# Optimization experiments

Measured on AMD Instinct MI355X. Metric: run time of the kernel, lower is better.

The kernel has to match this reference:

```python
import jax, jax.numpy as jnp
import numpy as np

N_NODES = 50000
N_EDGES = 800000
IN_FEATS = 128
OUT_FEATS = 128
HEADS = 2
EW_DIMS = 2
NEG_SLOPE = 0.2


def setup_inputs() -> dict:
    key = jax.random.key(0)
    ks = jax.random.split(key, 8)
    feat = jax.random.normal(ks[0], (N_NODES, IN_FEATS), dtype=jnp.float32)
    e_w = jax.random.uniform(ks[1], (N_EDGES, EW_DIMS), dtype=jnp.float32)
    src = jax.random.randint(ks[2], (N_EDGES,), 0, N_NODES)
    dst = jax.random.randint(ks[3], (N_EDGES,), 0, N_NODES)
    # Learned params: per-head fc weight, attn vectors (xavier-ish scale)
    s = 1.0 / np.sqrt(IN_FEATS)
    W = jax.random.normal(ks[4], (HEADS, OUT_FEATS, IN_FEATS), dtype=jnp.float32) * s
    attn_l = jax.random.normal(ks[5], (HEADS, OUT_FEATS), dtype=jnp.float32) * s
    attn_r = jax.random.normal(ks[6], (HEADS, OUT_FEATS), dtype=jnp.float32) * s
    attn_ew = jax.random.normal(ks[7], (HEADS, EW_DIMS), dtype=jnp.float32)
    return {"feat": feat, "e_w": e_w, "src": src, "dst": dst,
            "W": W, "attn_l": attn_l, "attn_r": attn_r, "attn_ew": attn_ew}


def reference(feat, e_w, src, dst, W, attn_l, attn_r, attn_ew):
    N = feat.shape[0]
    # per-head projection: [N, H, O]
    ft = jnp.einsum('nf,hof->nho', feat, W)
    el = jnp.einsum('nho,ho->nh', ft, attn_l)           # [N, H]
    er = jnp.einsum('nho,ho->nh', ft, attn_r)           # [N, H]
    ew = jnp.einsum('ed,hd->eh', e_w, attn_ew)          # [E, H]
    # u_add_v + edge-weight attention + leaky_relu
    e = jax.nn.leaky_relu(el[src] + er[dst] + ew, NEG_SLOPE)  # [E, H]
    # edge_softmax grouped by destination node (numerically stable)
    emax = jax.ops.segment_max(e, dst, num_segments=N)
    emax = jnp.where(jnp.isfinite(emax), emax, 0.0)
    ee = jnp.exp(e - emax[dst])
    denom = jax.ops.segment_sum(ee, dst, num_segments=N)
    a = ee / jnp.where(denom[dst] > 0, denom[dst], 1.0)       # [E, H]
    # u_mul_e / sum aggregation: [N, H, O]
    m = ft[src] * a[:, :, None]
    rst = jax.ops.segment_sum(m, dst, num_segments=N)
    # residual (Identity since in_feats == out_feats) + elu, then cat heads
    rst = jax.nn.elu(rst + feat[:, None, :])
    return rst.reshape(N, -1)
```

## Files before the change

### kernel.cpp

```cpp
#include <hip/hip_runtime.h>
#include <math.h>

#define NNODES 50000
#define NEDGES 800000
#define INF 128
#define OUTF 128
#define HEADS 2
#define NEG_SLOPE 0.2f

#define CAP 32
#define SCAP 16
#define OVFCAP 32768

__device__ __forceinline__ unsigned short f2bf(float f) {
    unsigned u = __float_as_uint(f);
    unsigned r = (u + 0x7FFFu + ((u >> 16) & 1u)) >> 16;
    return (unsigned short)r;
}
__device__ __forceinline__ float bf2f(unsigned short b) {
    return __uint_as_float((unsigned)b << 16);
}

typedef __attribute__((ext_vector_type(8))) short frag_ab;
typedef __attribute__((ext_vector_type(4))) float frag_cd;
typedef __attribute__((ext_vector_type(8))) unsigned short ushort8v;

#define APITCH 136

__global__ void init_kernel(int* cursor, int* ovfcnt,
                            const float* __restrict__ W,
                            const float* __restrict__ attn_l,
                            const float* __restrict__ attn_r,
                            unsigned short* __restrict__ Wb,
                            float* __restrict__ wfold, int N) {
    const int b = blockIdx.x, t = threadIdx.x;
    const int czblk = (2 * N + 255) >> 8;
    if (b < czblk) {
        int i = b * 256 + t;
        if (i < 2 * N) cursor[i] = 0;
        if (i == 0) *ovfcnt = 0;
        return;
    }
    if (b == czblk) {
        int h = t >> 7, f = t & 127;
        float sl = 0.f, sr = 0.f;
#pragma unroll 16
        for (int o = 0; o < 128; ++o) {
            float wv = W[(size_t)(h * 128 + o) * 128 + f];
            sl = fmaf(attn_l[h * 128 + o], wv, sl);
            sr = fmaf(attn_r[h * 128 + o], wv, sr);
        }
        wfold[h * 128 + f] = sl;
        wfold[(2 + h) * 128 + f] = sr;
        return;
    }
    int base = (b - czblk - 1) * 4096 + t * 16;
#pragma unroll
    for (int q = 0; q < 4; ++q) {
        float4 g = *(const float4*)(W + base + q * 4);
        ushort4 v; v.x = f2bf(g.x); v.y = f2bf(g.y); v.z = f2bf(g.z); v.w = f2bf(g.w);
        *(ushort4*)(Wb + base + q * 4) = v;
    }
}

__global__ __launch_bounds__(256) void gemm_mfma(const float* __restrict__ feat,
                                                 const unsigned short* __restrict__ Wb,
                                                 const float* __restrict__ wfold,
                                                 unsigned short* __restrict__ ftb,
                                                 float* __restrict__ el,
                                                 float* __restrict__ er,
                                                 int N) {
    __shared__ unsigned short Bs[256 * APITCH];
    const int t = threadIdx.x;
    const int w = t >> 6, lane = t & 63;
    const int m16 = lane & 15, quad = lane >> 4;
    const int n0 = blockIdx.x * 64;
    const int r = n0 + w * 16 + m16;
    const bool valid = r < N;

#pragma unroll
    for (int i = 0; i < 16; ++i) {
        int q = t + i * 256;
        int row = q >> 4, c = q & 15;
        ushort8v v = *(const ushort8v*)(Wb + row * 128 + c * 8);
        *(ushort8v*)(&Bs[row * APITCH + c * 8]) = v;
    }

    frag_ab af[4];
    float pd[4] = {0.f, 0.f, 0.f, 0.f};
#pragma unroll
    for (int kc = 0; kc < 4; ++kc) {
        const int cc = kc * 32 + quad * 8;
        float4 g0 = make_float4(0.f, 0.f, 0.f, 0.f), g1 = g0;
        if (valid) {
            g0 = *(const float4*)(feat + (size_t)r * INF + cc);
            g1 = *(const float4*)(feat + (size_t)r * INF + cc + 4);
        }
        frag_ab a;
        a[0] = (short)f2bf(g0.x); a[1] = (short)f2bf(g0.y);
        a[2] = (short)f2bf(g0.z); a[3] = (short)f2bf(g0.w);
        a[4] = (short)f2bf(g1.x); a[5] = (short)f2bf(g1.y);
        a[6] = (short)f2bf(g1.z); a[7] = (short)f2bf(g1.w);
        af[kc] = a;
#pragma unroll
        for (int vq = 0; vq < 4; ++vq) {
            float4 w0 = *(const float4*)(wfold + vq * 128 + cc);
            float4 w1 = *(const float4*)(wfold + vq * 128 + cc + 4);
            pd[vq] += g0.x * w0.x + g0.y * w0.y + g0.z * w0.z + g0.w * w0.w
                    + g1.x * w1.x + g1.y * w1.y + g1.z * w1.z + g1.w * w1.w;
        }
    }
#pragma unroll
    for (int m = 16; m < 64; m <<= 1)
#pragma unroll
        for (int vq = 0; vq < 4; ++vq) pd[vq] += __shfl_xor(pd[vq], m, 64);
    if (valid && quad == 0) {
        *(float2*)(el + (size_t)r * 2) = make_float2(pd[0], pd[1]);
        *(float2*)(er + (size_t)r * 2) = make_float2(pd[2], pd[3]);
    }

    __syncthreads();

#pragma unroll
    for (int jt = 0; jt < 4; ++jt) {
        frag_cd acc[4];
#pragma unroll
        for (int nt = 0; nt < 4; ++nt) acc[nt] = frag_cd{0.f, 0.f, 0.f, 0.f};
#pragma unroll
        for (int kc = 0; kc < 4; ++kc)
#pragma unroll
            for (int nt = 0; nt < 4; ++nt) {
                frag_ab bf = *(const frag_ab*)(&Bs[(jt * 64 + nt * 16 + m16) * APITCH
                                                   + kc * 32 + quad * 8]);
                acc[nt] = __builtin_amdgcn_mfma_f32_16x16x32_bf16(af[kc], bf, acc[nt], 0, 0, 0);
            }
#pragma unroll
        for (int nt = 0; nt < 4; ++nt) {
            const int gj = jt * 64 + nt * 16 + m16;
#pragma unroll
            for (int reg = 0; reg < 4; ++reg) {
                int gm = n0 + w * 16 + quad * 4 + reg;
                if (gm < N) ftb[(size_t)gm * 256 + gj] = f2bf(acc[nt][reg]);
            }
        }
    }
}

__global__ void edge_fused(const float* __restrict__ el, const float* __restrict__ er,
                           const float* __restrict__ e_w, const int* __restrict__ src,
                           const int* __restrict__ dst, const float* __restrict__ attn_ew,
                           int* __restrict__ cursor, int* __restrict__ ovfcnt,
                           uint2* __restrict__ edata, float4* __restrict__ ovf,
                           int N, int E) {
    int e = blockIdx.x * 256 + threadIdx.x;
    if (e >= E) return;
    int s = src[e], d = dst[e];
    float2 ew2 = *(const float2*)(e_w + (size_t)e * 2);
    float2 elv = *(const float2*)(el + (size_t)s * 2);
    float2 erv = *(const float2*)(er + (size_t)d * 2);
    float v0 = elv.x + erv.x + ew2.x * attn_ew[0] + ew2.y * attn_ew[1];
    float v1 = elv.y + erv.y + ew2.x * attn_ew[2] + ew2.y * attn_ew[3];
    v0 = v0 >= 0.f ? v0 : NEG_SLOPE * v0;
    v1 = v1 >= 0.f ? v1 : NEG_SLOPE * v1;
    float ee0 = __expf(v0);
    float ee1 = __expf(v1);
    unsigned pk = ((unsigned)f2bf(ee1) << 16) | (unsigned)f2bf(ee0);
    uint2 rec = make_uint2((unsigned)s, pk);
    uint2* bin = edata + (size_t)d * CAP;
    int sh = e & 1;
    int pos = atomicAdd(cursor + (size_t)sh * N + d, 1);
    if (pos < SCAP) {
        bin[sh * SCAP + pos] = rec;
    } else {
        sh ^= 1;
        int pos2 = atomicAdd(cursor + (size_t)sh * N + d, 1);
        if (pos2 < SCAP) {
            bin[sh * SCAP + pos2] = rec;
        } else {
            int o = atomicAdd(ovfcnt, 1);
            if (o < OVFCAP)
                ovf[o] = make_float4(__int_as_float(d), __int_as_float(s), ee0, ee1);
        }
    }
}

__global__ __launch_bounds__(256) void aggregate(const unsigned short* __restrict__ ftb,
                                                 const float* __restrict__ feat,
                                                 const uint2* __restrict__ edata,
                                                 const int* __restrict__ cursor,
                                                 const int* __restrict__ ovfcnt,
                                                 const float4* __restrict__ ovf,
                                                 float* __restrict__ out, int N) {
    const int t = threadIdx.x;
    const int w = t >> 6, l = t & 63;
    const int n = blockIdx.x * 4 + w;
    if (n >= N) return;
    const int hl = l & 31;
    const int half = l >> 5;
    const int c8 = 8 * hl;
    const int h = hl >> 4;
    const int c0c = cursor[n], c1c = cursor[N + n];
    const int cnt0 = c0c < SCAP ? c0c : SCAP;
    const int cnt1 = c1c < SCAP ? c1c : SCAP;
    const int cnt = cnt0 + cnt1;
    const uint2* eb = edata + (size_t)n * CAP;

    float4 a0 = make_float4(0.f, 0.f, 0.f, 0.f);
    float4 a1 = make_float4(0.f, 0.f, 0.f, 0.f);
    float dn = 0.f;
    const int hm = (cnt + 1) >> 1;
#pragma unroll 8
    for (int i = 0; i < hm; ++i) {
        const int j = 2 * i + half;
        const bool vld = j < cnt;
        const int jj = j < cnt0 ? j : j - cnt0 + SCAP;
        uint2 rec = eb[vld ? jj : 0];
        float aw = bf2f((unsigned short)(h ? (rec.y >> 16) : (rec.y & 0xFFFFu)));
        float a = vld ? aw : 0.f;
        unsigned su = vld ? rec.x : 0u;
        ushort8v v = *(const ushort8v*)(ftb + (size_t)su * 256 + c8);
        dn += a;
        a0.x = fmaf(a, bf2f(v[0]), a0.x);
        a0.y = fmaf(a, bf2f(v[1]), a0.y);
        a0.z = fmaf(a, bf2f(v[2]), a0.z);
        a0.w = fmaf(a, bf2f(v[3]), a0.w);
        a1.x = fmaf(a, bf2f(v[4]), a1.x);
        a1.y = fmaf(a, bf2f(v[5]), a1.y);
        a1.z = fmaf(a, bf2f(v[6]), a1.z);
        a1.w = fmaf(a, bf2f(v[7]), a1.w);
    }
    a0.x += __shfl_xor(a0.x, 32, 64);
    a0.y += __shfl_xor(a0.y, 32, 64);
    a0.z += __shfl_xor(a0.z, 32, 64);
    a0.w += __shfl_xor(a0.w, 32, 64);
    a1.x += __shfl_xor(a1.x, 32, 64);
    a1.y += __shfl_xor(a1.y, 32, 64);
    a1.z += __shfl_xor(a1.z, 32, 64);
    a1.w += __shfl_xor(a1.w, 32, 64);
    dn += __shfl_xor(dn, 32, 64);

    if (c0c > SCAP && c1c > SCAP) {
        int no = *ovfcnt; if (no > OVFCAP) no = OVFCAP;
        for (int i = 0; i < no; ++i) {
            float4 ov = ovf[i];
            if (__float_as_int(ov.x) == n) {
                int s = __float_as_int(ov.y);
                float a = h ? ov.w : ov.z;
                dn += a;
                ushort8v v = *(const ushort8v*)(ftb + (size_t)s * 256 + c8);
                a0.x = fmaf(a, bf2f(v[0]), a0.x);
                a0.y = fmaf(a, bf2f(v[1]), a0.y);
                a0.z = fmaf(a, bf2f(v[2]), a0.z);
                a0.w = fmaf(a, bf2f(v[3]), a0.w);
                a1.x = fmaf(a, bf2f(v[4]), a1.x);
                a1.y = fmaf(a, bf2f(v[5]), a1.y);
                a1.z = fmaf(a, bf2f(v[6]), a1.z);
                a1.w = fmaf(a, bf2f(v[7]), a1.w);
            }
        }
    }
    float inv = dn > 0.f ? 1.0f / dn : 0.f;
    const int cb = c8 + 4 * half;
    float4 av = half ? a1 : a0;
    float4 f4 = *(const float4*)(feat + (size_t)n * INF + (cb & 127));
    float4 r;
    r.x = fmaf(av.x, inv, f4.x);
    r.y = fmaf(av.y, inv, f4.y);
    r.z = fmaf(av.z, inv, f4.z);
    r.w = fmaf(av.w, inv, f4.w);
    r.x = r.x > 0.f ? r.x : expm1f(r.x);
    r.y = r.y > 0.f ? r.y : expm1f(r.y);
    r.z = r.z > 0.f ? r.z : expm1f(r.z);
    r.w = r.w > 0.f ? r.w : expm1f(r.w);
    *(float4*)(out + (size_t)n * 256 + cb) = r;
}

extern "C" void kernel_launch(void* const* d_in, const int* in_sizes, int n_in,
                              void* d_out, int out_size, void* d_ws, size_t ws_size,
                              hipStream_t stream) {
    const float* feat    = (const float*)d_in[0];
    const float* e_w     = (const float*)d_in[1];
    const int*   src     = (const int*)d_in[2];
    const int*   dst     = (const int*)d_in[3];
    const float* W       = (const float*)d_in[4];
    const float* attn_l  = (const float*)d_in[5];
    const float* attn_r  = (const float*)d_in[6];
    const float* attn_ew = (const float*)d_in[7];
    float* out = (float*)d_out;

    const int N = in_sizes[0] / INF;
    const int E = in_sizes[2];

    unsigned short* ftb = (unsigned short*)d_ws;
    uint2*  edata  = (uint2*)(ftb + (size_t)N * 256);
    float*  el     = (float*)(edata + (size_t)N * CAP);
    float*  er     = el + (size_t)N * 2;
    float*  wfold  = er + (size_t)N * 2;
    unsigned short* Wb = (unsigned short*)(wfold + 512);
    float4* ovf    = (float4*)(Wb + 32768);
    int*    cursor = (int*)(ovf + OVFCAP);
    int*    ovfcnt = cursor + 2 * (size_t)N;

    const int czblk = (2 * N + 255) / 256;
    init_kernel<<<czblk + 9, 256, 0, stream>>>(cursor, ovfcnt, W, attn_l, attn_r, Wb, wfold, N);

    gemm_mfma<<<(N + 63) / 64, 256, 0, stream>>>(feat, Wb, wfold, ftb, el, er, N);

    edge_fused<<<(E + 255) / 256, 256, 0, stream>>>(el, er, e_w, src, dst, attn_ew,
                                                    cursor, ovfcnt, edata, ovf, N, E);

    aggregate<<<(N + 3) / 4, 256, 0, stream>>>(ftb, feat, edata, cursor, ovfcnt, ovf, out, N);
}
```

Before: 224.6 us.

## Bin edges per XCD with workgroup-scope atomics, add compaction pass, widen GEMM tile

Measured after the change: 247.3 us. 10.1% more time.

```diff
diff --git a/kernel.cpp b/kernel.cpp
--- a/kernel.cpp
+++ b/kernel.cpp
@@ -8,9 +8,12 @@
 #define HEADS 2
 #define NEG_SLOPE 0.2f
 
-#define CAP 32
-#define SCAP 16
+#define NXCD 8
+#define SCAPX 8
+#define NSLOT 64
+#define DCAP 32
 #define OVFCAP 32768
+#define OVFFLAG 0x40000000
 
 __device__ __forceinline__ unsigned short f2bf(float f) {
     unsigned u = __float_as_uint(f);
@@ -20,6 +23,11 @@
 __device__ __forceinline__ float bf2f(unsigned short b) {
     return __uint_as_float((unsigned)b << 16);
 }
+__device__ __forceinline__ unsigned cvt_pk_bf16(float lo, float hi) {
+    unsigned r;
+    asm("v_cvt_pk_bf16_f32 %0, %1, %2" : "=v"(r) : "v"(lo), "v"(hi));
+    return r;
+}
 
 typedef __attribute__((ext_vector_type(8))) short frag_ab;
 typedef __attribute__((ext_vector_type(4))) float frag_cd;
@@ -27,21 +35,21 @@
 
 #define APITCH 136
 
-__global__ void init_kernel(int* cursor, int* ovfcnt,
+__global__ void init_kernel(int* cur8, int* ,
                             const float* __restrict__ W,
                             const float* __restrict__ attn_l,
                             const float* __restrict__ attn_r,
                             unsigned short* __restrict__ Wb,
                             float* __restrict__ wfold, int N) {
     const int b = blockIdx.x, t = threadIdx.x;
-    const int czblk = (2 * N + 255) >> 8;
-    if (b < czblk) {
+    const int zn = NXCD * N + 1;
+    const int zblk = (zn + 255) >> 8;
+    if (b < zblk) {
         int i = b * 256 + t;
-        if (i < 2 * N) cursor[i] = 0;
-        if (i == 0) *ovfcnt = 0;
+        if (i < zn) cur8[i] = 0;
         return;
     }
-    if (b == czblk) {
+    if (b == zblk) {
         int h = t >> 7, f = t & 127;
         float sl = 0.f, sr = 0.f;
 #pragma unroll 16
@@ -54,7 +62,7 @@
         wfold[(2 + h) * 128 + f] = sr;
         return;
     }
-    int base = (b - czblk - 1) * 4096 + t * 16;
+    int base = (b - zblk - 1) * 4096 + t * 16;
 #pragma unroll
     for (int q = 0; q < 4; ++q) {
         float4 g = *(const float4*)(W + base + q * 4);
@@ -74,9 +82,10 @@
     const int t = threadIdx.x;
     const int w = t >> 6, lane = t & 63;
     const int m16 = lane & 15, quad = lane >> 4;
-    const int n0 = blockIdx.x * 64;
-    const int r = n0 + w * 16 + m16;
-    const bool valid = r < N;
+    const int n0 = blockIdx.x * 128;
+    const int r0 = n0 + w * 16 + m16;
+    const int r1 = r0 + 64;
+    const bool v0 = r0 < N, v1 = r1 < N;
 
 #pragma unroll
     for (int i = 0; i < 16; ++i) {
@@ -86,74 +95,102 @@
         *(ushort8v*)(&Bs[row * APITCH + c * 8]) = v;
     }
 
-    frag_ab af[4];
-    float pd[4] = {0.f, 0.f, 0.f, 0.f};
+    frag_ab af[2][4];
+    float pd[2][4] = {{0.f, 0.f, 0.f, 0.f}, {0.f, 0.f, 0.f, 0.f}};
 #pragma unroll
     for (int kc = 0; kc < 4; ++kc) {
         const int cc = kc * 32 + quad * 8;
-        float4 g0 = make_float4(0.f, 0.f, 0.f, 0.f), g1 = g0;
-        if (valid) {
-            g0 = *(const float4*)(feat + (size_t)r * INF + cc);
-            g1 = *(const float4*)(feat + (size_t)r * INF + cc + 4);
-        }
-        frag_ab a;
-        a[0] = (short)f2bf(g0.x); a[1] = (short)f2bf(g0.y);
-        a[2] = (short)f2bf(g0.z); a[3] = (short)f2bf(g0.w);
-        a[4] = (short)f2bf(g1.x); a[5] = (short)f2bf(g1.y);
-        a[6] = (short)f2bf(g1.z); a[7] = (short)f2bf(g1.w);
-        af[kc] = a;
+        float4 ga0 = make_float4(0.f, 0.f, 0.f, 0.f), ga1 = ga0;
+        float4 gb0 = ga0, gb1 = ga0;
+        if (v0) {
+            ga0 = *(const float4*)(feat + (size_t)r0 * INF + cc);
+            ga1 = *(const float4*)(feat + (size_t)r0 * INF + cc + 4);
+        }
+        if (v1) {
+            gb0 = *(const float4*)(feat + (size_t)r1 * INF + cc);
+            gb1 = *(const float4*)(feat + (size_t)r1 * INF + cc + 4);
+        }
+        union { int4 i; frag_ab f; } ua, ub;
+        ua.i.x = (int)cvt_pk_bf16(ga0.x, ga0.y); ua.i.y = (int)cvt_pk_bf16(ga0.z, ga0.w);
+        ua.i.z = (int)cvt_pk_bf16(ga1.x, ga1.y); ua.i.w = (int)cvt_pk_bf16(ga1.z, ga1.w);
+        ub.i.x = (int)cvt_pk_bf16(gb0.x, gb0.y); ub.i.y = (int)cvt_pk_bf16(gb0.z, gb0.w);
+        ub.i.z = (int)cvt_pk_bf16(gb1.x, gb1.y); ub.i.w = (int)cvt_pk_bf16(gb1.z, gb1.w);
+        af[0][kc] = ua.f; af[1][kc] = ub.f;
 #pragma unroll
         for (int vq = 0; vq < 4; ++vq) {
             float4 w0 = *(const float4*)(wfold + vq * 128 + cc);
             float4 w1 = *(const float4*)(wfold + vq * 128 + cc + 4);
-            pd[vq] += g0.x * w0.x + g0.y * w0.y + g0.z * w0.z + g0.w * w0.w
-                    + g1.x * w1.x + g1.y * w1.y + g1.z * w1.z + g1.w * w1.w;
+            pd[0][vq] += ga0.x * w0.x + ga0.y * w0.y + ga0.z * w0.z + ga0.w * w0.w
+                       + ga1.x * w1.x + ga1.y * w1.y + ga1.z * w1.z + ga1.w * w1.w;
+            pd[1][vq] += gb0.x * w0.x + gb0.y * w0.y + gb0.z * w0.z + gb0.w * w0.w
+                       + gb1.x * w1.x + gb1.y * w1.y + gb1.z * w1.z + gb1.w * w1.w;
         }
     }
 #pragma unroll
     for (int m = 16; m < 64; m <<= 1)
 #pragma unroll
-        for (int vq = 0; vq < 4; ++vq) pd[vq] += __shfl_xor(pd[vq], m, 64);
-    if (valid && quad == 0) {
-        *(float2*)(el + (size_t)r * 2) = make_float2(pd[0], pd[1]);
-        *(float2*)(er + (size_t)r * 2) = make_float2(pd[2], pd[3]);
+        for (int rg = 0; rg < 2; ++rg)
+#pragma unroll
+            for (int vq = 0; vq < 4; ++vq) pd[rg][vq] += __shfl_xor(pd[rg][vq], m, 64);
+    if (quad == 0) {
+        if (v0) {
+            *(float2*)(el + (size_t)r0 * 2) = make_float2(pd[0][0], pd[0][1]);
+            *(float2*)(er + (size_t)r0 * 2) = make_float2(pd[0][2], pd[0][3]);
+        }
+        if (v1) {
+            *(float2*)(el + (size_t)r1 * 2) = make_float2(pd[1][0], pd[1][1]);
+            *(float2*)(er + (size_t)r1 * 2) = make_float2(pd[1][2], pd[1][3]);
+        }
     }
 
     __syncthreads();
 
-#pragma unroll
+#pragma unroll 1
     for (int jt = 0; jt < 4; ++jt) {
-        frag_cd acc[4];
-#pragma unroll
-        for (int nt = 0; nt < 4; ++nt) acc[nt] = frag_cd{0.f, 0.f, 0.f, 0.f};
+        frag_cd acc[2][4];
+#pragma unroll
+        for (int rg = 0; rg < 2; ++rg)
+#pragma unroll
+            for (int nt = 0; nt < 4; ++nt) acc[rg][nt] = frag_cd{0.f, 0.f, 0.f, 0.f};
 #pragma unroll
         for (int kc = 0; kc < 4; ++kc)
 #pragma unroll
             for (int nt = 0; nt < 4; ++nt) {
                 frag_ab bf = *(const frag_ab*)(&Bs[(jt * 64 + nt * 16 + m16) * APITCH
                                                    + kc * 32 + quad * 8]);
-                acc[nt] = __builtin_amdgcn_mfma_f32_16x16x32_bf16(af[kc], bf, acc[nt], 0, 0, 0);
+                acc[0][nt] = __builtin_amdgcn_mfma_f32_16x16x32_bf16(bf, af[0][kc],
+                                                                     acc[0][nt], 0, 0, 0);
+                acc[1][nt] = __builtin_amdgcn_mfma_f32_16x16x32_bf16(bf, af[1][kc],
+                                                                     acc[1][nt], 0, 0, 0);
             }
 #pragma unroll
-        for (int nt = 0; nt < 4; ++nt) {
-            const int gj = jt * 64 + nt * 16 + m16;
-#pragma unroll
-            for (int reg = 0; reg < 4; ++reg) {
-                int gm = n0 + w * 16 + quad * 4 + reg;
-                if (gm < N) ftb[(size_t)gm * 256 + gj] = f2bf(acc[nt][reg]);
+        for (int rg = 0; rg < 2; ++rg) {
+            const int rr = rg ? r1 : r0;
+            if (rg ? v1 : v0) {
+#pragma unroll
+                for (int nt = 0; nt < 4; ++nt) {
+                    uint2 p;
+                    p.x = cvt_pk_bf16(acc[rg][nt][0], acc[rg][nt][1]);
+                    p.y = cvt_pk_bf16(acc[rg][nt][2], acc[rg][nt][3]);
+                    *(uint2*)(ftb + (size_t)rr * 256 + jt * 64 + nt * 16 + quad * 4) = p;
+                }
             }
         }
     }
 }
 
-__global__ void edge_fused(const float* __restrict__ el, const float* __restrict__ er,
+__global__ __launch_bounds__(256) void edge_fused(const float* __restrict__ el,
+                           const float* __restrict__ er,
                            const float* __restrict__ e_w, const int* __restrict__ src,
                            const int* __restrict__ dst, const float* __restrict__ attn_ew,
-                           int* __restrict__ cursor, int* __restrict__ ovfcnt,
-                           uint2* __restrict__ edata, float4* __restrict__ ovf,
-                           int N, int E) {
+                           int* __restrict__ cur8, int* __restrict__ ovfcnt,
+                           uint2* __restrict__ bins, float4* __restrict__ ovf,
+                           int E) {
     int e = blockIdx.x * 256 + threadIdx.x;
     if (e >= E) return;
+    unsigned xcc;
+    asm volatile("s_getreg_b32 %0, hwreg(HW_REG_XCC_ID)" : "=s"(xcc));
+    xcc &= (NXCD - 1);
     int s = src[e], d = dst[e];
     float2 ew2 = *(const float2*)(e_w + (size_t)e * 2);
     float2 elv = *(const float2*)(el + (size_t)s * 2);
@@ -164,30 +201,54 @@
     v1 = v1 >= 0.f ? v1 : NEG_SLOPE * v1;
     float ee0 = __expf(v0);
     float ee1 = __expf(v1);
-    unsigned pk = ((unsigned)f2bf(ee1) << 16) | (unsigned)f2bf(ee0);
-    uint2 rec = make_uint2((unsigned)s, pk);
-    uint2* bin = edata + (size_t)d * CAP;
-    int sh = e & 1;
-    int pos = atomicAdd(cursor + (size_t)sh * N + d, 1);
-    if (pos < SCAP) {
-        bin[sh * SCAP + pos] = rec;
+    int pos = __hip_atomic_fetch_add(cur8 + (size_t)d * NXCD + xcc, 1,
+                                     __ATOMIC_RELAXED, __HIP_MEMORY_SCOPE_WORKGROUP);
+    if (pos < SCAPX) {
+        unsigned pk = ((unsigned)f2bf(ee1) << 16) | (unsigned)f2bf(ee0);
+        bins[(size_t)d * NSLOT + xcc * SCAPX + pos] = make_uint2((unsigned)s, pk);
     } else {
-        sh ^= 1;
-        int pos2 = atomicAdd(cursor + (size_t)sh * N + d, 1);
-        if (pos2 < SCAP) {
-            bin[sh * SCAP + pos2] = rec;
+        int o = atomicAdd(ovfcnt, 1);
+        if (o < OVFCAP)
+            ovf[o] = make_float4(__int_as_float(d), __int_as_float(s), ee0, ee1);
+    }
+}
+
+__global__ __launch_bounds__(256) void compact_bins(uint2* __restrict__ bins,
+                                                    const int* __restrict__ cur8,
+                                                    int* __restrict__ cntd,
+                                                    int* __restrict__ ovfcnt,
+                                                    float4* __restrict__ ovf, int N) {
+    const int t = threadIdx.x;
+    const int w = t >> 6, l = t & 63;
+    const int n = blockIdx.x * 4 + w;
+    if (n >= N) return;
+    const int x = l >> 3, slot = l & 7;
+    const int cx = cur8[(size_t)n * NXCD + x];
+    uint2 rec = bins[(size_t)n * NSLOT + l];
+    const int cxc = cx < SCAPX ? cx : SCAPX;
+    const bool valid = slot < cxc;
+    unsigned long long mask = __ballot(valid);
+    int pos = __popcll(mask & ((1ull << l) - 1ull));
+    int tot = __popcll(mask);
+    bool oflag = __any(slot == 0 && cx > SCAPX) || (tot > DCAP);
+    if (valid) {
+        if (pos < DCAP) {
+            bins[(size_t)n * NSLOT + pos] = rec;
         } else {
             int o = atomicAdd(ovfcnt, 1);
             if (o < OVFCAP)
-                ovf[o] = make_float4(__int_as_float(d), __int_as_float(s), ee0, ee1);
-        }
-    }
+                ovf[o] = make_float4(__int_as_float(n), __int_as_float((int)rec.x),
+                                     bf2f((unsigned short)(rec.y & 0xFFFFu)),
+                                     bf2f((unsigned short)(rec.y >> 16)));
+        }
+    }
+    if (l == 0) cntd[n] = (tot < DCAP ? tot : DCAP) | (oflag ? OVFFLAG : 0);
 }
 
 __global__ __launch_bounds__(256) void aggregate(const unsigned short* __restrict__ ftb,
                                                  const float* __restrict__ feat,
-                                                 const uint2* __restrict__ edata,
-                                                 const int* __restrict__ cursor,
+                                                 const uint2* __restrict__ bins,
+                                                 const int* __restrict__ cntd,
                                                  const int* __restrict__ ovfcnt,
                                                  const float4* __restrict__ ovf,
                                                  float* __restrict__ out, int N) {
@@ -199,11 +260,9 @@
     const int half = l >> 5;
     const int c8 = 8 * hl;
     const int h = hl >> 4;
-    const int c0c = cursor[n], c1c = cursor[N + n];
-    const int cnt0 = c0c < SCAP ? c0c : SCAP;
-    const int cnt1 = c1c < SCAP ? c1c : SCAP;
-    const int cnt = cnt0 + cnt1;
-    const uint2* eb = edata + (size_t)n * CAP;
+    const int cw = cntd[n];
+    const int cnt = cw & 0xFFFF;
+    const uint2* eb = bins + (size_t)n * NSLOT;
 
     float4 a0 = make_float4(0.f, 0.f, 0.f, 0.f);
     float4 a1 = make_float4(0.f, 0.f, 0.f, 0.f);
@@ -213,8 +272,7 @@
     for (int i = 0; i < hm; ++i) {
         const int j = 2 * i + half;
         const bool vld = j < cnt;
-        const int jj = j < cnt0 ? j : j - cnt0 + SCAP;
-        uint2 rec = eb[vld ? jj : 0];
+        uint2 rec = eb[vld ? j : 0];
         float aw = bf2f((unsigned short)(h ? (rec.y >> 16) : (rec.y & 0xFFFFu)));
         float a = vld ? aw : 0.f;
         unsigned su = vld ? rec.x : 0u;
@@ -239,7 +297,7 @@
     a1.w += __shfl_xor(a1.w, 32, 64);
     dn += __shfl_xor(dn, 32, 64);
 
-    if (c0c > SCAP && c1c > SCAP) {
+    if (cw & OVFFLAG) {
         int no = *ovfcnt; if (no > OVFCAP) no = OVFCAP;
         for (int i = 0; i < no; ++i) {
             float4 ov = ovf[i];
@@ -292,22 +350,25 @@
     const int E = in_sizes[2];
 
     unsigned short* ftb = (unsigned short*)d_ws;
-    uint2*  edata  = (uint2*)(ftb + (size_t)N * 256);
-    float*  el     = (float*)(edata + (size_t)N * CAP);
+    uint2*  bins   = (uint2*)(ftb + (size_t)N * 256);
+    float*  el     = (float*)(bins + (size_t)N * NSLOT);
     float*  er     = el + (size_t)N * 2;
     float*  wfold  = er + (size_t)N * 2;
     unsigned short* Wb = (unsigned short*)(wfold + 512);
     float4* ovf    = (float4*)(Wb + 32768);
-    int*    cursor = (int*)(ovf + OVFCAP);
-    int*    ovfcnt = cursor + 2 * (size_t)N;
-
-    const int czblk = (2 * N + 255) / 256;
-    init_kernel<<<czblk + 9, 256, 0, stream>>>(cursor, ovfcnt, W, attn_l, attn_r, Wb, wfold, N);
-
-    gemm_mfma<<<(N + 63) / 64, 256, 0, stream>>>(feat, Wb, wfold, ftb, el, er, N);
+    int*    cur8   = (int*)(ovf + OVFCAP);
+    int*    ovfcnt = cur8 + (size_t)NXCD * N;
+    int*    cntd   = ovfcnt + 1;
+
+    const int zblk = (NXCD * N + 1 + 255) / 256;
+    init_kernel<<<zblk + 9, 256, 0, stream>>>(cur8, ovfcnt, W, attn_l, attn_r, Wb, wfold, N);
+
+    gemm_mfma<<<(N + 127) / 128, 256, 0, stream>>>(feat, Wb, wfold, ftb, el, er, N);
 
     edge_fused<<<(E + 255) / 256, 256, 0, stream>>>(el, er, e_w, src, dst, attn_ew,
-                                                    cursor, ovfcnt, edata, ovf, N, E);
-
-    aggregate<<<(N + 3) / 4, 256, 0, stream>>>(ftb, feat, edata, cursor, ovfcnt, ovf, out, N);
-}
+                                                    cur8, ovfcnt, bins, ovf, E);
+
+    compact_bins<<<(N + 3) / 4, 256, 0, stream>>>(bins, cur8, cntd, ovfcnt, ovf, N);
+
+    aggregate<<<(N + 3) / 4, 256, 0, stream>>>(ftb, feat, bins, cntd, ovfcnt, ovf, out, N);
+}
```
